# Performance work log

Measured on AMD Instinct MI355X. Metric: run time of the kernel, lower is better.

Reference implementation:

```python
import jax, jax.numpy as jnp
import numpy as np

B, S, HID = 2, 2048, 2048
H, KV, D = 16, 8, 128
EPS = 1e-6
MROPE = [21, 21, 22]  # half_dim=64 -> [64//3, 64//3, 64-2*(64//3)]
SCALE = D ** -0.5


def setup_inputs() -> dict:
    key = jax.random.key(0)
    ks = jax.random.split(key, 8)
    hidden_states = jax.random.normal(ks[0], (B, S, HID), jnp.float32)
    # 3D mrope cos/sin: one position grid per modality axis (use same arange positions)
    inv_freq = 1.0 / (10000.0 ** (jnp.arange(0, D, 2, dtype=jnp.float32) / D))  # [64]
    pos = jnp.arange(S, dtype=jnp.float32)
    freqs = pos[:, None] * inv_freq[None, :]                  # [S, 64]
    emb = jnp.concatenate([freqs, freqs], axis=-1)            # [S, 128]
    cos = jnp.broadcast_to(jnp.cos(emb)[None, None], (3, B, S, D)).astype(jnp.float32)
    sin = jnp.broadcast_to(jnp.sin(emb)[None, None], (3, B, S, D)).astype(jnp.float32)
    q_w = jax.random.normal(ks[1], (H * D, HID), jnp.float32) * 0.02
    k_w = jax.random.normal(ks[2], (KV * D, HID), jnp.float32) * 0.02
    v_w = jax.random.normal(ks[3], (KV * D, HID), jnp.float32) * 0.02
    o_w = jax.random.normal(ks[4], (HID, H * D), jnp.float32) * 0.02
    q_norm_w = jnp.ones((D,), jnp.float32)
    k_norm_w = jnp.ones((D,), jnp.float32)
    return dict(hidden_states=hidden_states, cos=cos, sin=sin, q_w=q_w, k_w=k_w,
                v_w=v_w, o_w=o_w, q_norm_w=q_norm_w, k_norm_w=k_norm_w)


def _rmsnorm(x, w):
    var = jnp.mean(jnp.square(x.astype(jnp.float32)), axis=-1, keepdims=True)
    return (x * jax.lax.rsqrt(var + EPS)).astype(x.dtype) * w


def _rotate_half(x):
    x1, x2 = jnp.split(x, 2, axis=-1)
    return jnp.concatenate([-x2, x1], axis=-1)


def _mrope_mix(t):
    # t: [3, B, S, D]; split last dim into mrope_section*2 chunks, pick chunk i from axis-0 index i%3
    sections = MROPE * 2
    idx = np.cumsum(sections)[:-1]
    chunks = jnp.split(t, idx, axis=-1)
    mixed = jnp.concatenate([c[i % 3] for i, c in enumerate(chunks)], axis=-1)  # [B, S, D]
    return mixed[:, None, :, :]  # unsqueeze head dim -> [B, 1, S, D]


def reference(hidden_states, cos, sin, q_w, k_w, v_w, o_w, q_norm_w, k_norm_w):
    # QKV projections -> [B, n_heads, S, D]
    q = (hidden_states @ q_w.T).reshape(B, S, H, D)
    k = (hidden_states @ k_w.T).reshape(B, S, KV, D)
    v = (hidden_states @ v_w.T).reshape(B, S, KV, D)
    q = _rmsnorm(q, q_norm_w).transpose(0, 2, 1, 3)   # [B, H, S, D]
    k = _rmsnorm(k, k_norm_w).transpose(0, 2, 1, 3)   # [B, KV, S, D]
    v = v.transpose(0, 2, 1, 3)                       # [B, KV, S, D]
    # 3D multimodal RoPE
    c = _mrope_mix(cos)
    s = _mrope_mix(sin)
    q = q * c + _rotate_half(q) * s
    k = k * c + _rotate_half(k) * s
    # GQA: repeat kv heads
    groups = H // KV
    k = jnp.repeat(k, groups, axis=1)  # [B, H, S, D]
    v = jnp.repeat(v, groups, axis=1)
    # causal SDPA (eager)
    scores = jnp.einsum('bhqd,bhkd->bhqk', q, k) * SCALE
    causal = jnp.tril(jnp.ones((S, S), bool))
    scores = jnp.where(causal[None, None], scores, jnp.finfo(scores.dtype).min)
    probs = jax.nn.softmax(scores, axis=-1)
    attn = jnp.einsum('bhqk,bhkd->bhqd', probs, v)     # [B, H, S, D]
    attn = attn.transpose(0, 2, 1, 3).reshape(B, S, H * D)
    return attn @ o_w.T
```

## Files before the change

kernel.cpp:

```cpp
#include <hip/hip_runtime.h>
#include <hip/hip_bf16.h>

typedef __attribute__((ext_vector_type(8))) short short8;
typedef __attribute__((ext_vector_type(4))) short short4v;
typedef __attribute__((ext_vector_type(4))) float f32x4;

#define B_ 2
#define S_ 2048
#define HID_ 2048
#define H_ 16
#define KV_ 8
#define D_ 128
#define SCALE_ 0.08838834764831845f

__device__ inline short f2bf(float f) {
    union { __hip_bfloat16 h; short s; } u;
    u.h = __float2bfloat16(f);
    return u.s;
}
__device__ inline float bf2f(short s) {
    union { short s; __hip_bfloat16 h; } u;
    u.s = s;
    return __bfloat162float(u.h);
}

__device__ inline void gld16(const short* g, short* l) {
    __builtin_amdgcn_global_load_lds(
        (const __attribute__((address_space(1))) unsigned int*)g,
        (__attribute__((address_space(3))) unsigned int*)l, 16, 0, 0);
}

__device__ inline int mrope_axis(int d) {
    int m = d & 63;
    return m < 21 ? 0 : (m < 42 ? 1 : 2);
}
__global__ __launch_bounds__(256) void prep(const float* __restrict__ hid,
                                            const float* __restrict__ qw_,
                                            const float* __restrict__ kw_,
                                            const float* __restrict__ vw_,
                                            const float* __restrict__ ow_,
                                            const float* __restrict__ cosp,
                                            const float* __restrict__ sinp,
                                            short* __restrict__ Hb,
                                            short* __restrict__ Wqkv,
                                            short* __restrict__ Owb,
                                            float* __restrict__ cm,
                                            float* __restrict__ sm) {
    int bid = blockIdx.x;
    if (bid < 20480) {
        const float* src; short* dst; int base;
        if (bid < 8192)       { src = hid; dst = Hb;              base = bid; }
        else if (bid < 12288) { src = qw_; dst = Wqkv;            base = bid - 8192; }
        else if (bid < 14336) { src = kw_; dst = Wqkv + 4194304;  base = bid - 12288; }
        else if (bid < 16384) { src = vw_; dst = Wqkv + 6291456;  base = bid - 14336; }
        else                  { src = ow_; dst = Owb;             base = bid - 16384; }
        int i = base * 1024 + threadIdx.x * 4;
        float4 v = *(const float4*)(&src[i]);
        short4v o;
        o.x = f2bf(v.x); o.y = f2bf(v.y); o.z = f2bf(v.z); o.w = f2bf(v.w);
        *(short4v*)(&dst[i]) = o;
    } else {
        const size_t AX = (size_t)B_ * S_ * D_;
        int i0 = (bid - 20480) * 1024 + threadIdx.x * 4;
#pragma unroll
        for (int k = 0; k < 4; ++k) {
            int idx = i0 + k;
            int d = idx & (D_ - 1);
            size_t src = (size_t)mrope_axis(d) * AX + idx;
            cm[idx] = cosp[src];
            sm[idx] = sinp[src];
        }
    }
}

__global__ __launch_bounds__(256) void gemm_bt(const short* __restrict__ A,
                                               const short* __restrict__ B,
                                               float* __restrict__ C,
                                               int M, int N, int K) {
    __shared__ __align__(16) short As[128 * 64];
    __shared__ __align__(16) short Bs[128 * 64];
    int tid = threadIdx.x;
    int wave = tid >> 6, lane = tid & 63;
    int m16 = lane & 15, quad = lane >> 4;
    int wr = wave >> 1, wc = wave & 1;
    int m0 = blockIdx.y * 128, n0 = blockIdx.x * 128;
    int srow = lane >> 3;
    int scol = ((lane & 7) ^ srow) << 3;
    f32x4 acc[4][4] = {};
    for (int k0 = 0; k0 < K; k0 += 64) {
#pragma unroll
        for (int i = 0; i < 4; ++i) {
            gld16(&A[(size_t)(m0 + wave * 32 + i * 8 + srow) * K + k0 + scol],
                  &As[(wave * 32 + i * 8) * 64]);
            gld16(&B[(size_t)(n0 + wave * 32 + i * 8 + srow) * K + k0 + scol],
                  &Bs[(wave * 32 + i * 8) * 64]);
        }
        __syncthreads();
        short8 a[4][2], b[4][2];
#pragma unroll
        for (int i = 0; i < 4; ++i)
#pragma unroll
            for (int kk = 0; kk < 2; ++kk) {
                int gsw = (((kk << 2) + quad) ^ (m16 & 7)) << 3;
                a[i][kk] = *(const short8*)(&As[(wr * 64 + i * 16 + m16) * 64 + gsw]);
                b[i][kk] = *(const short8*)(&Bs[(wc * 64 + i * 16 + m16) * 64 + gsw]);
            }
#pragma unroll
        for (int kk = 0; kk < 2; ++kk)
#pragma unroll
            for (int i = 0; i < 4; ++i)
#pragma unroll
                for (int j = 0; j < 4; ++j)
                    acc[i][j] = __builtin_amdgcn_mfma_f32_16x16x32_bf16(a[i][kk], b[j][kk],
                                                                        acc[i][j], 0, 0, 0);
        __syncthreads();
    }
#pragma unroll
    for (int i = 0; i < 4; ++i) {
        int row = m0 + wr * 64 + i * 16 + quad * 4;
#pragma unroll
        for (int j = 0; j < 4; ++j) {
            int col = n0 + wc * 64 + j * 16 + m16;
#pragma unroll
            for (int r = 0; r < 4; ++r)
                C[(size_t)(row + r) * N + col] = acc[i][j][r];
        }
    }
}

#define TP 136
__global__ __launch_bounds__(256) void qkv_fused(const short* __restrict__ A,
                                                 const short* __restrict__ Bw,
                                                 const float* __restrict__ qnw,
                                                 const float* __restrict__ knw,
                                                 const float* __restrict__ cm,
                                                 const float* __restrict__ sm,
                                                 short* __restrict__ Qb,
                                                 short* __restrict__ Kb,
                                                 short* __restrict__ Vb) {
    __shared__ __align__(16) char smem[36864];
    short* As = (short*)smem;
    short* Bs = (short*)(smem + 16384);
    short* T  = (short*)smem;
    float* partial = (float*)(smem + 34816);
    float* rsA     = (float*)(smem + 35840);
    const int K = HID_;
    int tid = threadIdx.x;
    int wave = tid >> 6, lane = tid & 63;
    int m16 = lane & 15, quad = lane >> 4;
    int wr = wave >> 1, wc = wave & 1;
    int m0 = blockIdx.y * 128, n0 = blockIdx.x * 128;
    int hk = blockIdx.x;
    int srow = lane >> 3;
    int scol = ((lane & 7) ^ srow) << 3;
    f32x4 acc[4][4] = {};
    for (int k0 = 0; k0 < K; k0 += 64) {
#pragma unroll
        for (int i = 0; i < 4; ++i) {
            gld16(&A[(size_t)(m0 + wave * 32 + i * 8 + srow) * K + k0 + scol],
                  &As[(wave * 32 + i * 8) * 64]);
            gld16(&Bw[(size_t)(n0 + wave * 32 + i * 8 + srow) * K + k0 + scol],
                  &Bs[(wave * 32 + i * 8) * 64]);
        }
        __syncthreads();
        short8 a[4][2], b[4][2];
#pragma unroll
        for (int i = 0; i < 4; ++i)
#pragma unroll
            for (int kk = 0; kk < 2; ++kk) {
                int gsw = (((kk << 2) + quad) ^ (m16 & 7)) << 3;
                a[i][kk] = *(const short8*)(&As[(wr * 64 + i * 16 + m16) * 64 + gsw]);
                b[i][kk] = *(const short8*)(&Bs[(wc * 64 + i * 16 + m16) * 64 + gsw]);
            }
#pragma unroll
        for (int kk = 0; kk < 2; ++kk)
#pragma unroll
            for (int i = 0; i < 4; ++i)
#pragma unroll
                for (int j = 0; j < 4; ++j)
                    acc[i][j] = __builtin_amdgcn_mfma_f32_16x16x32_bf16(a[i][kk], b[j][kk],
                                                                        acc[i][j], 0, 0, 0);
        __syncthreads();
    }
    int b = m0 >> 11, s0 = m0 & (S_ - 1);
    if (hk >= 24) {
        int kv = hk - 24;
#pragma unroll
        for (int i = 0; i < 4; ++i)
#pragma unroll
            for (int j = 0; j < 4; ++j) {
                short4v v4;
#pragma unroll
                for (int r = 0; r < 4; ++r) v4[r] = f2bf(acc[i][j][r]);
                *(short4v*)&T[(wc * 64 + j * 16 + m16) * TP + wr * 64 + i * 16 + quad * 4] = v4;
            }
        __syncthreads();
        size_t vb = ((size_t)(b * KV_ + kv)) * D_;
#pragma unroll
        for (int it = 0; it < 8; ++it) {
            int e = (it * 256 + tid) * 8;
            int dcol = e >> 7, srw = e & 127;
            *(short8*)&Vb[(vb + dcol) * S_ + s0 + srw] = *(const short8*)&T[dcol * TP + srw];
        }
    } else {
#pragma unroll
        for (int i = 0; i < 4; ++i)
#pragma unroll
            for (int r = 0; r < 4; ++r) {
                float t = 0.f;
#pragma unroll
                for (int j = 0; j < 4; ++j) t += acc[i][j][r] * acc[i][j][r];
#pragma unroll
                for (int msk = 8; msk >= 1; msk >>= 1) t += __shfl_xor(t, msk, 64);
                if (m16 == 0) partial[wc * 128 + wr * 64 + i * 16 + quad * 4 + r] = t;
            }
#pragma unroll
        for (int i = 0; i < 4; ++i)
#pragma unroll
            for (int j = 0; j < 4; ++j)
#pragma unroll
                for (int r = 0; r < 4; ++r)
                    T[(wr * 64 + i * 16 + quad * 4 + r) * TP + wc * 64 + j * 16 + m16] =
                        f2bf(acc[i][j][r]);
        __syncthreads();
        if (tid < 128) {
            float tot = partial[tid] + partial[128 + tid];
            rsA[tid] = rsqrtf(tot * (1.0f / 128.0f) + 1e-6f);
        }
        __syncthreads();
        const float* nw = (hk < 16) ? qnw : knw;
        short* outp = (hk < 16) ? (Qb + ((size_t)(b * H_ + hk)) * S_ * D_)
                                : (Kb + ((size_t)(b * KV_ + hk - 16)) * S_ * D_);
        size_t cmb = ((size_t)(b * S_ + s0)) * D_;
#pragma unroll
        for (int it = 0; it < 8; ++it) {
            int e = (it * 256 + tid) * 8;
            int row = e >> 7, colc = e & 127;
            int pc = colc ^ 64;
            float rs = rsA[row];
            float sg = (colc < 64) ? -1.f : 1.f;
            short8 nv = *(const short8*)&T[row * TP + colc];
            short8 pv = *(const short8*)&T[row * TP + pc];
            float4 cA = *(const float4*)&cm[cmb + (size_t)row * D_ + colc];
            float4 cB = *(const float4*)&cm[cmb + (size_t)row * D_ + colc + 4];
            float4 sA = *(const float4*)&sm[cmb + (size_t)row * D_ + colc];
            float4 sB = *(const float4*)&sm[cmb + (size_t)row * D_ + colc + 4];
            float4 wA = *(const float4*)&nw[colc];
            float4 wB = *(const float4*)&nw[colc + 4];
            float4 wpA = *(const float4*)&nw[pc];
            float4 wpB = *(const float4*)&nw[pc + 4];
            float cs[8] = {cA.x, cA.y, cA.z, cA.w, cB.x, cB.y, cB.z, cB.w};
            float sn[8] = {sA.x, sA.y, sA.z, sA.w, sB.x, sB.y, sB.z, sB.w};
            float wv[8] = {wA.x, wA.y, wA.z, wA.w, wB.x, wB.y, wB.z, wB.w};
            float wp[8] = {wpA.x, wpA.y, wpA.z, wpA.w, wpB.x, wpB.y, wpB.z, wpB.w};
            short8 o;
#pragma unroll
            for (int k = 0; k < 8; ++k) {
                float x = bf2f(nv[k]) * rs * wv[k];
                float p = bf2f(pv[k]) * rs * wp[k];
                o[k] = f2bf(x * cs[k] + sg * p * sn[k]);
            }
            *(short8*)&outp[(size_t)(s0 + row) * D_ + colc] = o;
        }
    }
}

#define KPAD 136
#define VPAD 72
__global__ __launch_bounds__(256) void attn_fa(const short* __restrict__ Qb,
                                               const short* __restrict__ Kb,
                                               const short* __restrict__ Vb,
                                               short* __restrict__ Ab) {
    __shared__ __align__(16) short Ks[64 * KPAD];
    __shared__ __align__(16) short Vs[128 * VPAD];
    __shared__ __align__(16) short Ps[4][16 * VPAD];
    int tid = threadIdx.x;
    int wave = tid >> 6, lane = tid & 63;
    int m16 = lane & 15, quad = lane >> 4;
    int bh = blockIdx.x;
    int h = bh & 15, b = bh >> 4;
    int qt = 31 - blockIdx.y;
    int kv = h >> 1;
    const short* Qp = Qb + (size_t)(b * H_ + h) * S_ * D_;
    const short* Kp = Kb + (size_t)(b * KV_ + kv) * S_ * D_;
    const short* Vp = Vb + (size_t)(b * KV_ + kv) * D_ * S_;
    int q_base = qt * 64 + wave * 16;
    int qrow = q_base + m16;
    short8 qf[4];
#pragma unroll
    for (int c = 0; c < 4; ++c)
        qf[c] = *(const short8*)(&Qp[(size_t)(q_base + m16) * D_ + c * 32 + quad * 8]);
    f32x4 o_acc[8] = {};
    float m_r = -1e30f, l_r = 0.f;
    int nchunks = qt + 1;
    for (int kc = 0; kc < nchunks; ++kc) {
        int k0 = kc * 64;
#pragma unroll
        for (int it = 0; it < 4; ++it) {
            int cc = tid + it * 256;
            int row = cc >> 4, col = (cc & 15) * 8;
            *(uint4*)(&Ks[row * KPAD + col]) = *(const uint4*)(&Kp[(size_t)(k0 + row) * D_ + col]);
        }
#pragma unroll
        for (int it = 0; it < 4; ++it) {
            int cc = tid + it * 256;
            int row = cc >> 3, col = (cc & 7) * 8;
            *(uint4*)(&Vs[row * VPAD + col]) = *(const uint4*)(&Vp[(size_t)row * S_ + k0 + col]);
        }
        __syncthreads();
        float sv[4][4];
#pragma unroll
        for (int nt = 0; nt < 4; ++nt) {
            f32x4 facc = {};
#pragma unroll
            for (int c = 0; c < 4; ++c) {
                short8 kfr = *(const short8*)(&Ks[(nt * 16 + m16) * KPAD + c * 32 + quad * 8]);
                facc = __builtin_amdgcn_mfma_f32_16x16x32_bf16(kfr, qf[c], facc, 0, 0, 0);
            }
            if (kc == qt) {
#pragma unroll
                for (int r = 0; r < 4; ++r) {
                    int key = k0 + nt * 16 + quad * 4 + r;
                    sv[nt][r] = (key <= qrow) ? facc[r] * SCALE_ : -1e30f;
                }
            } else {
#pragma unroll
                for (int r = 0; r < 4; ++r) sv[nt][r] = facc[r] * SCALE_;
            }
        }
        float mx = -1e30f;
#pragma unroll
        for (int nt = 0; nt < 4; ++nt)
#pragma unroll
            for (int r = 0; r < 4; ++r) mx = fmaxf(mx, sv[nt][r]);
        mx = fmaxf(mx, __shfl_xor(mx, 16, 64));
        mx = fmaxf(mx, __shfl_xor(mx, 32, 64));
        float m_new = fmaxf(m_r, mx);
        float alpha = __expf(m_r - m_new);
        float p[4][4], sum = 0.f;
#pragma unroll
        for (int nt = 0; nt < 4; ++nt)
#pragma unroll
            for (int r = 0; r < 4; ++r) { p[nt][r] = __expf(sv[nt][r] - m_new); sum += p[nt][r]; }
        sum += __shfl_xor(sum, 16, 64);
        sum += __shfl_xor(sum, 32, 64);
        l_r = l_r * alpha + sum;
        m_r = m_new;
#pragma unroll
        for (int j = 0; j < 8; ++j) {
            f32x4 t = o_acc[j];
#pragma unroll
            for (int r = 0; r < 4; ++r) t[r] *= alpha;
            o_acc[j] = t;
        }
#pragma unroll
        for (int nt = 0; nt < 4; ++nt) {
            short4v pk;
#pragma unroll
            for (int r = 0; r < 4; ++r) pk[r] = f2bf(p[nt][r]);
            *(short4v*)&Ps[wave][m16 * VPAD + nt * 16 + quad * 4] = pk;
        }
#pragma unroll
        for (int kk = 0; kk < 2; ++kk) {
            short8 pf = *(const short8*)(&Ps[wave][m16 * VPAD + kk * 32 + quad * 8]);
#pragma unroll
            for (int j = 0; j < 8; ++j) {
                short8 vfr = *(const short8*)(&Vs[(j * 16 + m16) * VPAD + kk * 32 + quad * 8]);
                o_acc[j] = __builtin_amdgcn_mfma_f32_16x16x32_bf16(vfr, pf, o_acc[j], 0, 0, 0);
            }
        }
        __syncthreads();
    }
    float inv_l = 1.0f / l_r;
    size_t base = ((size_t)(b * S_ + qrow)) * (H_ * D_) + h * D_;
#pragma unroll
    for (int j = 0; j < 8; ++j) {
        short4v ov;
#pragma unroll
        for (int r = 0; r < 4; ++r) ov[r] = f2bf(o_acc[j][r] * inv_l);
        *(short4v*)&Ab[base + j * 16 + quad * 4] = ov;
    }
}

extern "C" void kernel_launch(void* const* d_in, const int* in_sizes, int n_in,
                              void* d_out, int out_size, void* d_ws, size_t ws_size,
                              hipStream_t stream) {
    const float* hid  = (const float*)d_in[0];
    const float* cosp = (const float*)d_in[1];
    const float* sinp = (const float*)d_in[2];
    const float* q_w  = (const float*)d_in[3];
    const float* k_w  = (const float*)d_in[4];
    const float* v_w  = (const float*)d_in[5];
    const float* o_w  = (const float*)d_in[6];
    const float* qnw  = (const float*)d_in[7];
    const float* knw  = (const float*)d_in[8];

    char* w = (char*)d_ws;
    short* Hb    = (short*)w;  w += (size_t)4096 * 2048 * 2;
    short* Wqkv  = (short*)w;  w += (size_t)4096 * 2048 * 2;
    short* Owb   = (short*)w;  w += (size_t)2048 * 2048 * 2;
    short* Qb    = (short*)w;  w += (size_t)B_ * H_ * S_ * D_ * 2;
    short* Kb    = (short*)w;  w += (size_t)B_ * KV_ * S_ * D_ * 2;
    short* Vb    = (short*)w;  w += (size_t)B_ * KV_ * D_ * S_ * 2;
    short* Ab    = (short*)w;  w += (size_t)4096 * 2048 * 2;
    float* cos_m = (float*)w;  w += (size_t)B_ * S_ * D_ * 4;
    float* sin_m = (float*)w;  w += (size_t)B_ * S_ * D_ * 4;

    prep<<<20992, 256, 0, stream>>>(hid, q_w, k_w, v_w, o_w, cosp, sinp,
                                    Hb, Wqkv, Owb, cos_m, sin_m);

    qkv_fused<<<dim3(32, 32), 256, 0, stream>>>(Hb, Wqkv, qnw, knw, cos_m, sin_m,
                                                Qb, Kb, Vb);

    attn_fa<<<dim3(32, 32), 256, 0, stream>>>(Qb, Kb, Vb, Ab);

    gemm_bt<<<dim3(16, 32), 256, 0, stream>>>(Ab, Owb, (float*)d_out, 4096, 2048, 2048);
}
```

Before: 349.4 us.

## Rewrite QKV GEMM as 256x256 double-buffered pipelined kernel with 8 waves

The fused QKV projection kernel moves from 128x128 tiles with 4 waves and one sync per k-step to 256x256 tiles with 8 waves and a 128KB double-buffered LDS ring. Global-to-LDS loads for the next k-slice are interleaved with MFMA phases using explicit waitcnt, sched barriers and setprio. The epilogue is restructured to handle two heads per block in two half passes. The intent is to raise data reuse and overlap memory with compute. The cost is only 256 blocks and heavy LDS use, which limits occupancy, plus more complex hand-scheduled code.

```diff
diff --git a/kernel.cpp b/kernel.cpp
--- a/kernel.cpp
+++ b/kernel.cpp
@@ -128,142 +128,219 @@
     }
 }
 
-#define TP 136
-__global__ __launch_bounds__(256) void qkv_fused(const short* __restrict__ A,
-                                                 const short* __restrict__ Bw,
-                                                 const float* __restrict__ qnw,
-                                                 const float* __restrict__ knw,
-                                                 const float* __restrict__ cm,
-                                                 const float* __restrict__ sm,
-                                                 short* __restrict__ Qb,
-                                                 short* __restrict__ Kb,
-                                                 short* __restrict__ Vb) {
-    __shared__ __align__(16) char smem[36864];
-    short* As = (short*)smem;
-    short* Bs = (short*)(smem + 16384);
-    short* T  = (short*)smem;
-    float* partial = (float*)(smem + 34816);
-    float* rsA     = (float*)(smem + 35840);
-    const int K = HID_;
+
+#define VM2 asm volatile("s_waitcnt vmcnt(2)" ::: "memory")
+#define VM0 asm volatile("s_waitcnt vmcnt(0)" ::: "memory")
+
+#define LDA(dst, QI)                                                               \
+    _Pragma("unroll") for (int ii = 0; ii < 4; ++ii)                               \
+        _Pragma("unroll") for (int kk = 0; kk < 2; ++kk)                           \
+            dst[ii][kk] = *(const short8*)&lds[RA +                                \
+                (wr * 128 + ((QI) * 4 + ii) * 16 + m16) * 64 +                     \
+                ((((kk << 2) + quad) ^ (m16 & 7)) << 3)]
+
+#define LDB(dst, QJ)                                                               \
+    _Pragma("unroll") for (int jj = 0; jj < 2; ++jj)                               \
+        _Pragma("unroll") for (int kk = 0; kk < 2; ++kk)                           \
+            dst[jj][kk] = *(const short8*)&lds[RB +                                \
+                ((QJ) * 128 + wc * 32 + jj * 16 + m16) * 64 +                      \
+                ((((kk << 2) + quad) ^ (m16 & 7)) << 3)]
+
+#define MM(ua, ub, QI, QJ)                                                         \
+    _Pragma("unroll") for (int kk = 0; kk < 2; ++kk)                               \
+        _Pragma("unroll") for (int ii = 0; ii < 4; ++ii)                           \
+            _Pragma("unroll") for (int jj = 0; jj < 2; ++jj)                       \
+                acc[(QI) * 4 + ii][(QJ) * 2 + jj] =                                \
+                    __builtin_amdgcn_mfma_f32_16x16x32_bf16(                       \
+                        ua[ii][kk], ub[jj][kk],                                    \
+                        acc[(QI) * 4 + ii][(QJ) * 2 + jj], 0, 0, 0)
+
+#define STGA(q) do {                                                               \
+    int r_ = (wave << 3) + (lane >> 3);                                            \
+    int g_ = (lane & 7) ^ (r_ & 7);                                                \
+    gld16(&Am[(size_t)(m0 + (q) * 64 + r_) * 2048 + kc + (g_ << 3)],               \
+          &lds[PA + (q) * 4096 + (wave << 9)]);                                    \
+} while (0)
+#define STGB(h, c) do {                                                            \
+    int s_ = (wave << 3) + (lane >> 3);                                            \
+    int sl_ = (h) * 128 + (c) * 64 + s_;                                           \
+    int rr_ = ((sl_ >> 5) & 3) * 64 + (h) * 32 + (sl_ & 31);                       \
+    int g_ = (lane & 7) ^ (sl_ & 7);                                               \
+    gld16(&Bm[(size_t)(n0 + rr_) * 2048 + kc + (g_ << 3)],                         \
+          &lds[PB + ((h) * 128 + (c) * 64) * 64 + (wave << 9)]);                   \
+} while (0)
+
+#define PH(LOADS, STG, MFMAS, WAITOP) do {                                         \
+    LOADS;                                                                         \
+    STG;                                                                           \
+    __builtin_amdgcn_sched_barrier(0);                                             \
+    __builtin_amdgcn_s_barrier();                                                  \
+    asm volatile("s_waitcnt lgkmcnt(0)" ::: "memory");                             \
+    __builtin_amdgcn_sched_barrier(0);                                             \
+    __builtin_amdgcn_s_setprio(1);                                                 \
+    MFMAS;                                                                         \
+    __builtin_amdgcn_s_setprio(0);                                                 \
+    WAITOP;                                                                        \
+    __builtin_amdgcn_sched_barrier(0);                                             \
+    __builtin_amdgcn_s_barrier();                                                  \
+} while (0)
+
+__global__ __launch_bounds__(512, 2) void qkv_fused(const short* __restrict__ Am,
+                                                    const short* __restrict__ Bm,
+                                                    const float* __restrict__ qnw,
+                                                    const float* __restrict__ knw,
+                                                    const float* __restrict__ cm,
+                                                    const float* __restrict__ sm,
+                                                    short* __restrict__ Qb,
+                                                    short* __restrict__ Kb,
+                                                    short* __restrict__ Vb) {
+    __shared__ __align__(16) char smem[131072];
+    short* lds = (short*)smem;
     int tid = threadIdx.x;
     int wave = tid >> 6, lane = tid & 63;
     int m16 = lane & 15, quad = lane >> 4;
-    int wr = wave >> 1, wc = wave & 1;
-    int m0 = blockIdx.y * 128, n0 = blockIdx.x * 128;
-    int hk = blockIdx.x;
-    int srow = lane >> 3;
-    int scol = ((lane & 7) ^ srow) << 3;
-    f32x4 acc[4][4] = {};
-    for (int k0 = 0; k0 < K; k0 += 64) {
-#pragma unroll
-        for (int i = 0; i < 4; ++i) {
-            gld16(&A[(size_t)(m0 + wave * 32 + i * 8 + srow) * K + k0 + scol],
-                  &As[(wave * 32 + i * 8) * 64]);
-            gld16(&Bw[(size_t)(n0 + wave * 32 + i * 8 + srow) * K + k0 + scol],
-                  &Bs[(wave * 32 + i * 8) * 64]);
-        }
-        __syncthreads();
-        short8 a[4][2], b[4][2];
-#pragma unroll
-        for (int i = 0; i < 4; ++i)
-#pragma unroll
-            for (int kk = 0; kk < 2; ++kk) {
-                int gsw = (((kk << 2) + quad) ^ (m16 & 7)) << 3;
-                a[i][kk] = *(const short8*)(&As[(wr * 64 + i * 16 + m16) * 64 + gsw]);
-                b[i][kk] = *(const short8*)(&Bs[(wc * 64 + i * 16 + m16) * 64 + gsw]);
-            }
-#pragma unroll
-        for (int kk = 0; kk < 2; ++kk)
-#pragma unroll
-            for (int i = 0; i < 4; ++i)
-#pragma unroll
-                for (int j = 0; j < 4; ++j)
-                    acc[i][j] = __builtin_amdgcn_mfma_f32_16x16x32_bf16(a[i][kk], b[j][kk],
-                                                                        acc[i][j], 0, 0, 0);
-        __syncthreads();
-    }
-    int b = m0 >> 11, s0 = m0 & (S_ - 1);
-    if (hk >= 24) {
-        int kv = hk - 24;
-#pragma unroll
-        for (int i = 0; i < 4; ++i)
-#pragma unroll
-            for (int j = 0; j < 4; ++j) {
-                short4v v4;
-#pragma unroll
-                for (int r = 0; r < 4; ++r) v4[r] = f2bf(acc[i][j][r]);
-                *(short4v*)&T[(wc * 64 + j * 16 + m16) * TP + wr * 64 + i * 16 + quad * 4] = v4;
-            }
-        __syncthreads();
-        size_t vb = ((size_t)(b * KV_ + kv)) * D_;
-#pragma unroll
-        for (int it = 0; it < 8; ++it) {
-            int e = (it * 256 + tid) * 8;
-            int dcol = e >> 7, srw = e & 127;
-            *(short8*)&Vb[(vb + dcol) * S_ + s0 + srw] = *(const short8*)&T[dcol * TP + srw];
+    int wr = wave >> 2, wc = wave & 3;
+    int m0 = blockIdx.y * 256, n0 = blockIdx.x * 256;
+    f32x4 acc[8][4] = {};
+
+    {
+        const int kc = 0, PA = 0, PB = 16384;
+        STGA(0); STGA(1); STGA(2); STGA(3);
+        STGB(0, 0); STGB(0, 1); STGB(1, 0); STGB(1, 1);
+        asm volatile("s_waitcnt vmcnt(0)" ::: "memory");
+        __builtin_amdgcn_sched_barrier(0);
+        __builtin_amdgcn_s_barrier();
+    }
+
+    short8 af[4][2], bfX[2][2], bfY[2][2];
+    for (int t = 0; t < 31; ++t) {
+        const int RA = (t & 1) << 15, RB = RA + 16384;
+        const int PA = RA ^ 32768, PB = PA + 16384;
+        const int kc = (t + 1) << 6;
+        PH({ LDA(af, 0); LDB(bfX, 0); }, { STGA(0); STGA(2); },       MM(af, bfX, 0, 0), VM2);
+        PH({ LDB(bfY, 1); },             { STGB(0, 0); STGB(0, 1); }, MM(af, bfY, 0, 1), );
+        PH({ LDA(af, 1); },              { STGB(1, 0); STGB(1, 1); }, MM(af, bfY, 1, 1), );
+        PH({ ; },                        { STGA(1); STGA(3); },       MM(af, bfX, 1, 0), VM2);
+    }
+    {
+        const int RA = 32768, RB = RA + 16384;
+        PH({ LDA(af, 0); LDB(bfX, 0); }, { ; }, MM(af, bfX, 0, 0), VM0);
+        PH({ LDB(bfY, 1); },             { ; }, MM(af, bfY, 0, 1), );
+        PH({ LDA(af, 1); },              { ; }, MM(af, bfY, 1, 1), );
+        PH({ ; },                        { ; }, MM(af, bfX, 1, 0), );
+    }
+
+    int bb = m0 >> 11, s0 = m0 & (S_ - 1);
+    int x = blockIdx.x;
+    if (x >= 12) {
+        short* T = (short*)smem;
+        int kv0 = (x - 12) << 1;
+        for (int hs = 0; hs < 2; ++hs) {
+            __syncthreads();
+            if (wr == hs) {
+#pragma unroll
+                for (int i = 0; i < 8; ++i)
+#pragma unroll
+                    for (int j = 0; j < 4; ++j) {
+                        short4v v4;
+#pragma unroll
+                        for (int r = 0; r < 4; ++r) v4[r] = f2bf(acc[i][j][r]);
+                        *(short4v*)&T[(wc * 64 + j * 16 + m16) * 136 + i * 16 + quad * 4] = v4;
+                    }
+            }
+            __syncthreads();
+#pragma unroll
+            for (int it = 0; it < 8; ++it) {
+                int e = (it * 512 + tid) * 8;
+                int col = e >> 7, ro = e & 127;
+                int kvh = col >> 7, d = col & 127;
+                *(short8*)&Vb[(((size_t)(bb * KV_ + kv0 + kvh)) * D_ + d) * S_ +
+                              s0 + hs * 128 + ro] =
+                    *(const short8*)&T[col * 136 + ro];
+            }
         }
     } else {
-#pragma unroll
-        for (int i = 0; i < 4; ++i)
-#pragma unroll
-            for (int r = 0; r < 4; ++r) {
-                float t = 0.f;
-#pragma unroll
-                for (int j = 0; j < 4; ++j) t += acc[i][j][r] * acc[i][j][r];
-#pragma unroll
-                for (int msk = 8; msk >= 1; msk >>= 1) t += __shfl_xor(t, msk, 64);
-                if (m16 == 0) partial[wc * 128 + wr * 64 + i * 16 + quad * 4 + r] = t;
-            }
-#pragma unroll
-        for (int i = 0; i < 4; ++i)
-#pragma unroll
-            for (int j = 0; j < 4; ++j)
-#pragma unroll
-                for (int r = 0; r < 4; ++r)
-                    T[(wr * 64 + i * 16 + quad * 4 + r) * TP + wc * 64 + j * 16 + m16] =
-                        f2bf(acc[i][j][r]);
-        __syncthreads();
-        if (tid < 128) {
-            float tot = partial[tid] + partial[128 + tid];
-            rsA[tid] = rsqrtf(tot * (1.0f / 128.0f) + 1e-6f);
-        }
-        __syncthreads();
-        const float* nw = (hk < 16) ? qnw : knw;
-        short* outp = (hk < 16) ? (Qb + ((size_t)(b * H_ + hk)) * S_ * D_)
-                                : (Kb + ((size_t)(b * KV_ + hk - 16)) * S_ * D_);
-        size_t cmb = ((size_t)(b * S_ + s0)) * D_;
-#pragma unroll
-        for (int it = 0; it < 8; ++it) {
-            int e = (it * 256 + tid) * 8;
-            int row = e >> 7, colc = e & 127;
-            int pc = colc ^ 64;
-            float rs = rsA[row];
-            float sg = (colc < 64) ? -1.f : 1.f;
-            short8 nv = *(const short8*)&T[row * TP + colc];
-            short8 pv = *(const short8*)&T[row * TP + pc];
-            float4 cA = *(const float4*)&cm[cmb + (size_t)row * D_ + colc];
-            float4 cB = *(const float4*)&cm[cmb + (size_t)row * D_ + colc + 4];
-            float4 sA = *(const float4*)&sm[cmb + (size_t)row * D_ + colc];
-            float4 sB = *(const float4*)&sm[cmb + (size_t)row * D_ + colc + 4];
-            float4 wA = *(const float4*)&nw[colc];
-            float4 wB = *(const float4*)&nw[colc + 4];
-            float4 wpA = *(const float4*)&nw[pc];
-            float4 wpB = *(const float4*)&nw[pc + 4];
-            float cs[8] = {cA.x, cA.y, cA.z, cA.w, cB.x, cB.y, cB.z, cB.w};
-            float sn[8] = {sA.x, sA.y, sA.z, sA.w, sB.x, sB.y, sB.z, sB.w};
-            float wv[8] = {wA.x, wA.y, wA.z, wA.w, wB.x, wB.y, wB.z, wB.w};
-            float wp[8] = {wpA.x, wpA.y, wpA.z, wpA.w, wpB.x, wpB.y, wpB.z, wpB.w};
-            short8 o;
-#pragma unroll
-            for (int k = 0; k < 8; ++k) {
-                float x = bf2f(nv[k]) * rs * wv[k];
-                float p = bf2f(pv[k]) * rs * wp[k];
-                o[k] = f2bf(x * cs[k] + sg * p * sn[k]);
-            }
-            *(short8*)&outp[(size_t)(s0 + row) * D_ + colc] = o;
-        }
-    }
-}
+        short* T = (short*)smem;
+        float* part = (float*)(smem + 67584);
+        float* rsL  = (float*)(smem + 69632);
+        const float* nw = (x < 8) ? qnw : knw;
+        int hbase = (x < 8) ? (x << 1) : ((x - 8) << 1);
+        short* obase = (x < 8) ? (Qb + ((size_t)bb * H_ + hbase) * S_ * D_)
+                               : (Kb + ((size_t)bb * KV_ + hbase) * S_ * D_);
+        for (int hs = 0; hs < 2; ++hs) {
+            __syncthreads();
+            if (wr == hs) {
+#pragma unroll
+                for (int i = 0; i < 8; ++i)
+#pragma unroll
+                    for (int r = 0; r < 4; ++r) {
+                        float t = acc[i][0][r] * acc[i][0][r] + acc[i][1][r] * acc[i][1][r]
+                                + acc[i][2][r] * acc[i][2][r] + acc[i][3][r] * acc[i][3][r];
+#pragma unroll
+                        for (int msk = 8; msk >= 1; msk >>= 1) t += __shfl_xor(t, msk, 64);
+                        if (m16 == 0) part[wc * 128 + i * 16 + quad * 4 + r] = t;
+                    }
+#pragma unroll
+                for (int i = 0; i < 8; ++i)
+#pragma unroll
+                    for (int j = 0; j < 4; ++j)
+#pragma unroll
+                        for (int r = 0; r < 4; ++r)
+                            T[(i * 16 + quad * 4 + r) * 264 + wc * 64 + j * 16 + m16] =
+                                f2bf(acc[i][j][r]);
+            }
+            __syncthreads();
+            if (tid < 256) {
+                int row = tid >> 1, hh = tid & 1;
+                float tot = part[hh * 256 + row] + part[hh * 256 + 128 + row];
+                rsL[tid] = rsqrtf(tot * (1.0f / 128.0f) + 1e-6f);
+            }
+            __syncthreads();
+#pragma unroll
+            for (int it = 0; it < 8; ++it) {
+                int e = (it * 512 + tid) * 8;
+                int row = e >> 8, c = e & 255;
+                int hh = c >> 7, colc = c & 127;
+                int pcol = colc ^ 64;
+                int srow = s0 + hs * 128 + row;
+                float rsv = rsL[row * 2 + hh];
+                float sg = (colc < 64) ? -1.f : 1.f;
+                short8 nv = *(const short8*)&T[row * 264 + c];
+                short8 pv = *(const short8*)&T[row * 264 + hh * 128 + pcol];
+                size_t cmb = ((size_t)(bb * S_ + srow)) * D_ + colc;
+                float4 cA = *(const float4*)&cm[cmb];
+                float4 cB = *(const float4*)&cm[cmb + 4];
+                float4 sA = *(const float4*)&sm[cmb];
+                float4 sB = *(const float4*)&sm[cmb + 4];
+                float4 wA = *(const float4*)&nw[colc];
+                float4 wB = *(const float4*)&nw[colc + 4];
+                float4 wpA = *(const float4*)&nw[pcol];
+                float4 wpB = *(const float4*)&nw[pcol + 4];
+                float cs[8] = {cA.x, cA.y, cA.z, cA.w, cB.x, cB.y, cB.z, cB.w};
+                float sn[8] = {sA.x, sA.y, sA.z, sA.w, sB.x, sB.y, sB.z, sB.w};
+                float wv[8] = {wA.x, wA.y, wA.z, wA.w, wB.x, wB.y, wB.z, wB.w};
+                float wp[8] = {wpA.x, wpA.y, wpA.z, wpA.w, wpB.x, wpB.y, wpB.z, wpB.w};
+                short8 o;
+#pragma unroll
+                for (int k = 0; k < 8; ++k) {
+                    float xv = bf2f(nv[k]) * rsv * wv[k];
+                    float pvv = bf2f(pv[k]) * rsv * wp[k];
+                    o[k] = f2bf(xv * cs[k] + sg * pvv * sn[k]);
+                }
+                *(short8*)&(obase + (size_t)hh * S_ * D_)[(size_t)srow * D_ + colc] = o;
+            }
+        }
+    }
+}
+
+#undef PH
+#undef LDA
+#undef LDB
+#undef MM
+#undef STGA
+#undef STGB
+#undef VM2
+#undef VM0
 
 #define KPAD 136
 #define VPAD 72
@@ -409,7 +486,7 @@
     prep<<<20992, 256, 0, stream>>>(hid, q_w, k_w, v_w, o_w, cosp, sinp,
                                     Hb, Wqkv, Owb, cos_m, sin_m);
 
-    qkv_fused<<<dim3(32, 32), 256, 0, stream>>>(Hb, Wqkv, qnw, knw, cos_m, sin_m,
+    qkv_fused<<<dim3(16, 16), 512, 0, stream>>>(Hb, Wqkv, qnw, knw, cos_m, sin_m,
                                                 Qb, Kb, Vb);
 
     attn_fa<<<dim3(32, 32), 256, 0, stream>>>(Qb, Kb, Vb, Ab);
```

Measured after the change: 353.1 us. About the same (+1.0%).

## Prefetch next K/V chunk into registers and raise wave priority around MFMA

Applied to the files above, without the earlier changes.

The attention loop now loads the next K and V chunk from global memory into registers while the current chunk is computed, then writes them to shared memory at the start of the next iteration. This hides global load latency behind the MFMA work. It also wraps the QK and PV MFMA sections in s_setprio raises and moves the P store to shared memory ahead of the accumulator rescale. The costs are 32 extra VGPRs per thread, which may lower occupancy, and a redundant load of chunk 0 on the last iteration.

```diff
diff --git a/kernel.cpp b/kernel.cpp
--- a/kernel.cpp
+++ b/kernel.cpp
@@ -293,22 +293,51 @@
     f32x4 o_acc[8] = {};
     float m_r = -1e30f, l_r = 0.f;
     int nchunks = qt + 1;
+
+    uint4 kreg[4], vreg[4];
+#pragma unroll
+    for (int it = 0; it < 4; ++it) {
+        int cc = tid + it * 256;
+        int row = cc >> 4, col = (cc & 15) * 8;
+        kreg[it] = *(const uint4*)(&Kp[(size_t)row * D_ + col]);
+    }
+#pragma unroll
+    for (int it = 0; it < 4; ++it) {
+        int cc = tid + it * 256;
+        int row = cc >> 3, col = (cc & 7) * 8;
+        vreg[it] = *(const uint4*)(&Vp[(size_t)row * S_ + col]);
+    }
+
     for (int kc = 0; kc < nchunks; ++kc) {
         int k0 = kc * 64;
 #pragma unroll
         for (int it = 0; it < 4; ++it) {
             int cc = tid + it * 256;
             int row = cc >> 4, col = (cc & 15) * 8;
-            *(uint4*)(&Ks[row * KPAD + col]) = *(const uint4*)(&Kp[(size_t)(k0 + row) * D_ + col]);
+            *(uint4*)(&Ks[row * KPAD + col]) = kreg[it];
         }
 #pragma unroll
         for (int it = 0; it < 4; ++it) {
             int cc = tid + it * 256;
             int row = cc >> 3, col = (cc & 7) * 8;
-            *(uint4*)(&Vs[row * VPAD + col]) = *(const uint4*)(&Vp[(size_t)row * S_ + k0 + col]);
+            *(uint4*)(&Vs[row * VPAD + col]) = vreg[it];
+        }
+        int nk0 = (kc + 1 < nchunks) ? (kc + 1) * 64 : 0;
+#pragma unroll
+        for (int it = 0; it < 4; ++it) {
+            int cc = tid + it * 256;
+            int row = cc >> 4, col = (cc & 15) * 8;
+            kreg[it] = *(const uint4*)(&Kp[(size_t)(nk0 + row) * D_ + col]);
+        }
+#pragma unroll
+        for (int it = 0; it < 4; ++it) {
+            int cc = tid + it * 256;
+            int row = cc >> 3, col = (cc & 7) * 8;
+            vreg[it] = *(const uint4*)(&Vp[(size_t)row * S_ + nk0 + col]);
         }
         __syncthreads();
         float sv[4][4];
+        __builtin_amdgcn_s_setprio(1);
 #pragma unroll
         for (int nt = 0; nt < 4; ++nt) {
             f32x4 facc = {};
@@ -328,6 +357,7 @@
                 for (int r = 0; r < 4; ++r) sv[nt][r] = facc[r] * SCALE_;
             }
         }
+        __builtin_amdgcn_s_setprio(0);
         float mx = -1e30f;
 #pragma unroll
         for (int nt = 0; nt < 4; ++nt)
@@ -347,19 +377,20 @@
         l_r = l_r * alpha + sum;
         m_r = m_new;
 #pragma unroll
+        for (int nt = 0; nt < 4; ++nt) {
+            short4v pk;
+#pragma unroll
+            for (int r = 0; r < 4; ++r) pk[r] = f2bf(p[nt][r]);
+            *(short4v*)&Ps[wave][m16 * VPAD + nt * 16 + quad * 4] = pk;
+        }
+#pragma unroll
         for (int j = 0; j < 8; ++j) {
             f32x4 t = o_acc[j];
 #pragma unroll
             for (int r = 0; r < 4; ++r) t[r] *= alpha;
             o_acc[j] = t;
         }
-#pragma unroll
-        for (int nt = 0; nt < 4; ++nt) {
-            short4v pk;
-#pragma unroll
-            for (int r = 0; r < 4; ++r) pk[r] = f2bf(p[nt][r]);
-            *(short4v*)&Ps[wave][m16 * VPAD + nt * 16 + quad * 4] = pk;
-        }
+        __builtin_amdgcn_s_setprio(1);
 #pragma unroll
         for (int kk = 0; kk < 2; ++kk) {
             short8 pf = *(const short8*)(&Ps[wave][m16 * VPAD + kk * 32 + quad * 8]);
@@ -369,6 +400,7 @@
                 o_acc[j] = __builtin_amdgcn_mfma_f32_16x16x32_bf16(vfr, pf, o_acc[j], 0, 0, 0);
             }
         }
+        __builtin_amdgcn_s_setprio(0);
         __syncthreads();
     }
     float inv_l = 1.0f / l_r;
```

After: 466.7 us. 1.34x slower.

## Double-buffer K/V tiles with direct global-to-LDS loads and XOR swizzle

Applied to the files above, without the earlier changes.

The attention kernel now keeps two LDS buffers for K and V. It prefetches the next chunk with direct global-to-LDS loads (gld16) while the current chunk is computed, and replaces padded layouts with an XOR-swizzled unpadded layout. It also raises wave priority around the MFMA sections and moves the P store ahead of the rescale. The aim is to hide global load latency and avoid bank conflicts. The cost is doubled LDS use, which may lower occupancy. Correctness also depends on how gld16 completion is waited on, since only one barrier per iteration remains.

```diff
diff --git a/kernel.cpp b/kernel.cpp
--- a/kernel.cpp
+++ b/kernel.cpp
@@ -265,14 +265,13 @@
     }
 }
 
-#define KPAD 136
 #define VPAD 72
 __global__ __launch_bounds__(256) void attn_fa(const short* __restrict__ Qb,
                                                const short* __restrict__ Kb,
                                                const short* __restrict__ Vb,
                                                short* __restrict__ Ab) {
-    __shared__ __align__(16) short Ks[64 * KPAD];
-    __shared__ __align__(16) short Vs[128 * VPAD];
+    __shared__ __align__(16) short Ks[2][64 * 128];
+    __shared__ __align__(16) short Vs[2][128 * 64];
     __shared__ __align__(16) short Ps[4][16 * VPAD];
     int tid = threadIdx.x;
     int wave = tid >> 6, lane = tid & 63;
@@ -293,28 +292,52 @@
     f32x4 o_acc[8] = {};
     float m_r = -1e30f, l_r = 0.f;
     int nchunks = qt + 1;
+
+#pragma unroll
+    for (int j = 0; j < 4; ++j) {
+        int idx = wave * 4 + j;
+        int r = idx * 4 + (lane >> 4);
+        int g = (lane & 15) ^ (r & 7);
+        gld16(&Kp[(size_t)r * D_ + g * 8], &Ks[0][idx * 512]);
+    }
+#pragma unroll
+    for (int j = 0; j < 4; ++j) {
+        int idx = wave * 4 + j;
+        int r = idx * 8 + (lane >> 3);
+        int g = (lane & 7) ^ (r & 7);
+        gld16(&Vp[(size_t)r * S_ + g * 8], &Vs[0][idx * 512]);
+    }
+    __syncthreads();
+
     for (int kc = 0; kc < nchunks; ++kc) {
         int k0 = kc * 64;
-#pragma unroll
-        for (int it = 0; it < 4; ++it) {
-            int cc = tid + it * 256;
-            int row = cc >> 4, col = (cc & 15) * 8;
-            *(uint4*)(&Ks[row * KPAD + col]) = *(const uint4*)(&Kp[(size_t)(k0 + row) * D_ + col]);
-        }
-#pragma unroll
-        for (int it = 0; it < 4; ++it) {
-            int cc = tid + it * 256;
-            int row = cc >> 3, col = (cc & 7) * 8;
-            *(uint4*)(&Vs[row * VPAD + col]) = *(const uint4*)(&Vp[(size_t)row * S_ + k0 + col]);
-        }
-        __syncthreads();
+        int cur = kc & 1;
+        if (kc + 1 < nchunks) {
+            int nk0 = k0 + 64, nb = cur ^ 1;
+#pragma unroll
+            for (int j = 0; j < 4; ++j) {
+                int idx = wave * 4 + j;
+                int r = idx * 4 + (lane >> 4);
+                int g = (lane & 15) ^ (r & 7);
+                gld16(&Kp[(size_t)(nk0 + r) * D_ + g * 8], &Ks[nb][idx * 512]);
+            }
+#pragma unroll
+            for (int j = 0; j < 4; ++j) {
+                int idx = wave * 4 + j;
+                int r = idx * 8 + (lane >> 3);
+                int g = (lane & 7) ^ (r & 7);
+                gld16(&Vp[(size_t)r * S_ + nk0 + g * 8], &Vs[nb][idx * 512]);
+            }
+        }
         float sv[4][4];
+        __builtin_amdgcn_s_setprio(1);
 #pragma unroll
         for (int nt = 0; nt < 4; ++nt) {
             f32x4 facc = {};
 #pragma unroll
             for (int c = 0; c < 4; ++c) {
-                short8 kfr = *(const short8*)(&Ks[(nt * 16 + m16) * KPAD + c * 32 + quad * 8]);
+                short8 kfr = *(const short8*)(&Ks[cur][(nt * 16 + m16) * 128 +
+                                                      ((((c << 2) + quad) ^ (m16 & 7)) << 3)]);
                 facc = __builtin_amdgcn_mfma_f32_16x16x32_bf16(kfr, qf[c], facc, 0, 0, 0);
             }
             if (kc == qt) {
@@ -328,6 +351,7 @@
                 for (int r = 0; r < 4; ++r) sv[nt][r] = facc[r] * SCALE_;
             }
         }
+        __builtin_amdgcn_s_setprio(0);
         float mx = -1e30f;
 #pragma unroll
         for (int nt = 0; nt < 4; ++nt)
@@ -347,28 +371,31 @@
         l_r = l_r * alpha + sum;
         m_r = m_new;
 #pragma unroll
+        for (int nt = 0; nt < 4; ++nt) {
+            short4v pk;
+#pragma unroll
+            for (int r = 0; r < 4; ++r) pk[r] = f2bf(p[nt][r]);
+            *(short4v*)&Ps[wave][m16 * VPAD + nt * 16 + quad * 4] = pk;
+        }
+#pragma unroll
         for (int j = 0; j < 8; ++j) {
             f32x4 t = o_acc[j];
 #pragma unroll
             for (int r = 0; r < 4; ++r) t[r] *= alpha;
             o_acc[j] = t;
         }
-#pragma unroll
-        for (int nt = 0; nt < 4; ++nt) {
-            short4v pk;
-#pragma unroll
-            for (int r = 0; r < 4; ++r) pk[r] = f2bf(p[nt][r]);
-            *(short4v*)&Ps[wave][m16 * VPAD + nt * 16 + quad * 4] = pk;
-        }
+        __builtin_amdgcn_s_setprio(1);
 #pragma unroll
         for (int kk = 0; kk < 2; ++kk) {
             short8 pf = *(const short8*)(&Ps[wave][m16 * VPAD + kk * 32 + quad * 8]);
 #pragma unroll
             for (int j = 0; j < 8; ++j) {
-                short8 vfr = *(const short8*)(&Vs[(j * 16 + m16) * VPAD + kk * 32 + quad * 8]);
+                short8 vfr = *(const short8*)(&Vs[cur][(j * 16 + m16) * 64 +
+                                                       ((((kk << 2) + quad) ^ (m16 & 7)) << 3)]);
                 o_acc[j] = __builtin_amdgcn_mfma_f32_16x16x32_bf16(vfr, pf, o_acc[j], 0, 0, 0);
             }
         }
+        __builtin_amdgcn_s_setprio(0);
         __syncthreads();
     }
     float inv_l = 1.0f / l_r;
```

Result: faster. 340.5 us (-2.6%).
